# Performance work log

Measured on AMD Instinct MI355X. Metric: run time of the kernel, lower is better.

The kernel has to match this reference:

```python
import jax, jax.numpy as jnp
import numpy as np

B, NG, C, H = 16, 1024, 768, 12
CAP = 16  # fixed routing capacity in gpu_pair (8 box slots from 0 up, 8 cls slots from 15 down)


def layernorm(x, g, b, eps=1e-5):
    m = x.mean(-1, keepdims=True)
    v = jnp.mean((x - m) ** 2, axis=-1, keepdims=True)
    return (x - m) * jax.lax.rsqrt(v + eps) * g + b


def setup_inputs() -> dict:
    key = jax.random.key(0)
    ks = jax.random.split(key, 8)
    s = 0.02
    return {
        "general_token": jax.random.normal(ks[0], (B, NG, C), jnp.float32),
        "cls_token": jax.random.normal(ks[1], (B, 1, C), jnp.float32),
        "box_token": jax.random.normal(ks[2], (B, 1, C), jnp.float32),
        "w_qkv": jax.random.normal(ks[3], (3 * C, C), jnp.float32) * s,
        "w_proj": jax.random.normal(ks[4], (C, C), jnp.float32) * s,
        "b_proj": jnp.zeros((C,), jnp.float32),
        "gamma1": jnp.ones((C,), jnp.float32),
        "beta1": jnp.zeros((C,), jnp.float32),
    }


def _route(sum_a, is_box):
    """On-device replication of gpu_pair's serial CPU loop for slots 0..15.

    Tokens are processed in descending sum_attn order; box-preferred tokens fill
    slots 0,1,2,..., cls-preferred tokens fill slots 15,14,13,.... Each category's
    writer per slot is unique; on a box/cls collision the later (larger sorted
    position) write wins, matching the serial loop's overwrite semantics. Slots
    never written stay 0 (np.zeros init). Wrapped-around writes (rank >= 16) land
    outside slots 0..15 in the original and are irrelevant to the output.
    """
    ng = sum_a.shape[0]
    perm = jnp.argsort(-sum_a)                      # descending sort
    ib = is_box[perm]
    ibi = ib.astype(jnp.int32)
    box_rank = jnp.cumsum(ibi) - ibi                # exclusive prefix count of box tokens
    cls_rank = jnp.cumsum(1 - ibi) - (1 - ibi)      # exclusive prefix count of cls tokens
    j = jnp.arange(ng, dtype=jnp.int32)
    box_pos = jnp.where(ib & (box_rank < CAP), box_rank, CAP)
    cls_pos = jnp.where((~ib) & (cls_rank < CAP), (CAP - 1) - cls_rank, CAP)
    empty = jnp.full((CAP,), -1, jnp.int32)
    box_j = empty.at[box_pos].set(j, mode='drop')   # unique writer per slot
    cls_j = empty.at[cls_pos].set(j, mode='drop')
    win = jnp.maximum(box_j, cls_j)
    return jnp.where(win >= 0, perm[jnp.maximum(win, 0)], 0)


def reference(general_token, cls_token, box_token, w_qkv, w_proj, b_proj, gamma1, beta1):
    # cat order in torch: cat(cls, cat(box, general)) -> [cls, box, general]
    cat = jnp.concatenate([cls_token, box_token, general_token], axis=1)  # [B,N,C]
    Bq, N, Cq = cat.shape
    hd = Cq // H
    x = layernorm(cat, gamma1, beta1)
    qkv = (x @ w_qkv.T).reshape(Bq, N, 3, H, hd).transpose(2, 0, 3, 1, 4)
    q, k, v = qkv[0], qkv[1], qkv[2]
    attn = jnp.einsum('bhnd,bhmd->bhnm', q, k) * (hd ** -0.5)
    # raw scores between cls<->box zeroed BEFORE softmax (not -inf)
    attn = attn.at[:, :, 0, 1].set(0.0).at[:, :, 1, 0].set(0.0)
    attn = jax.nn.softmax(attn, axis=-1)
    out = jnp.einsum('bhnm,bhmd->bhnd', attn, v).transpose(0, 2, 1, 3).reshape(Bq, N, Cq)
    out = out @ w_proj.T + b_proj
    cat = cat + out  # residual (drop_path identity in eval)
    cls_t, box_t, gen = cat[:, 0:1], cat[:, 1:2], cat[:, 2:]
    cls_attn = attn[:, :, 0, 2:].mean(axis=1)  # [B, N-2]
    box_attn = attn[:, :, 1, 2:].mean(axis=1)
    idx = jax.vmap(_route)(cls_attn + box_attn, box_attn > cls_attn)  # [B,16]
    gathered = jnp.take_along_axis(gen, idx[:, :, None], axis=1)      # [B,16,C]
    cls_task_token = jnp.concatenate([cls_t, gathered[:, 0:8]], axis=1)   # [B,9,C]
    box_task_token = jnp.concatenate([box_t, gathered[:, 8:16]], axis=1)  # [B,9,C]
    return cls_task_token, box_task_token
```

## Files before the change

kernel.cpp:

```cpp
#include <hip/hip_runtime.h>
#include <math.h>

namespace {

constexpr int Bn = 16;
constexpr int NG = 1024;
constexpr int Cc = 768;
constexpr int Hh = 12;
constexpr int HD = 64;
constexpr int Nn = 1026;
constexpr int NR = 18;
constexpr int NPK = 1152;
constexpr int NCH = 24;

typedef __attribute__((ext_vector_type(8))) short short8;
typedef __attribute__((ext_vector_type(4))) float f32x4;

__device__ inline unsigned short f2bf(float f) {
  unsigned u = __float_as_uint(f);
  unsigned r = u + 0x7FFFu + ((u >> 16) & 1u);
  return (unsigned short)(r >> 16);
}

__global__ __launch_bounds__(256) void k_ln(
    const float* __restrict__ gen, const float* __restrict__ cls,
    const float* __restrict__ box, const float* __restrict__ gamma,
    const float* __restrict__ beta, float* __restrict__ x,
    unsigned short* __restrict__ xbf) {
  int blk = blockIdx.x;
  int b = blk / Nn, n = blk % Nn;
  const float* src = (n == 0) ? cls + (size_t)b * Cc
                   : (n == 1) ? box + (size_t)b * Cc
                              : gen + ((size_t)b * NG + (n - 2)) * Cc;
  int t = threadIdx.x;
  float v0 = src[t], v1 = src[t + 256], v2 = src[t + 512];
  __shared__ double red[8];
  double s = (double)v0 + (double)v1 + (double)v2;
  for (int o = 32; o > 0; o >>= 1) s += __shfl_down(s, o, 64);
  int wid = t >> 6, lid = t & 63;
  if (lid == 0) red[wid] = s;
  __syncthreads();
  if (t == 0) red[4] = (red[0] + red[1] + red[2] + red[3]) / Cc;
  __syncthreads();
  double mean = red[4];
  double d0 = (double)v0 - mean, d1 = (double)v1 - mean, d2 = (double)v2 - mean;
  double sq = d0 * d0 + d1 * d1 + d2 * d2;
  for (int o = 32; o > 0; o >>= 1) sq += __shfl_down(sq, o, 64);
  __syncthreads();
  if (lid == 0) red[wid] = sq;
  __syncthreads();
  if (t == 0) {
    double var = (red[0] + red[1] + red[2] + red[3]) / Cc;
    red[5] = 1.0 / sqrt(var + 1e-5);
  }
  __syncthreads();
  double rs = red[5];
  float* dst = x + ((size_t)b * Nn + n) * Cc;
  unsigned short* dbf = xbf + ((size_t)b * NPK + n) * Cc;
  float o0 = (float)(d0 * rs * (double)gamma[t]       + (double)beta[t]);
  float o1 = (float)(d1 * rs * (double)gamma[t + 256] + (double)beta[t + 256]);
  float o2 = (float)(d2 * rs * (double)gamma[t + 512] + (double)beta[t + 512]);
  dst[t] = o0; dst[t + 256] = o1; dst[t + 512] = o2;
  dbf[t] = f2bf(o0); dbf[t + 256] = f2bf(o1); dbf[t + 512] = f2bf(o2);
}

__global__ __launch_bounds__(256) void k_padzero(unsigned short* __restrict__ xbf) {
  constexpr int PERB = (NPK - Nn) * Cc / 2;
  int idx = blockIdx.x * 256 + threadIdx.x;
  int total = Bn * PERB;
  for (int i = idx; i < total; i += gridDim.x * 256) {
    int b = i / PERB, r = i % PERB;
    unsigned int* p = (unsigned int*)(xbf + ((size_t)b * NPK + Nn) * Cc);
    p[r] = 0u;
  }
}

__global__ __launch_bounds__(256) void k_xt(
    const unsigned short* __restrict__ xbf, unsigned short* __restrict__ xT) {
  int b = blockIdx.x, jt = blockIdx.y, ct = blockIdx.z;
  int j0 = jt * 64, c0 = ct * 64;
  __shared__ unsigned short ts[64][80];
  int t = threadIdx.x;
  #pragma unroll
  for (int l = 0; l < 2; l++) {
    int chunk = t + l * 256;
    int r = chunk >> 3, c8 = chunk & 7;
    uint4 v = *(const uint4*)(xbf + ((size_t)b * NPK + j0 + r) * Cc + c0 + c8 * 8);
    *(uint4*)&ts[r][c8 * 8] = v;
  }
  __syncthreads();
  #pragma unroll
  for (int l = 0; l < 2; l++) {
    int chunk = t + l * 256;
    int orow = chunk >> 3, j8 = chunk & 7;
    unsigned short tmp[8];
    #pragma unroll
    for (int i = 0; i < 8; i++) tmp[i] = ts[j8 * 8 + i][orow];
    *(uint4*)(xT + ((size_t)b * Cc + c0 + orow) * NPK + j0 + j8 * 8) = *(uint4*)tmp;
  }
}

__global__ __launch_bounds__(256) void k_wcvt(
    const float* __restrict__ wqkv, const float* __restrict__ wproj,
    unsigned short* __restrict__ wqb, unsigned short* __restrict__ wvb,
    unsigned short* __restrict__ wpb) {
  int i = (blockIdx.x * 256 + threadIdx.x) * 4;
  if (i >= Cc * Cc) return;
  const float* wq = wqkv;
  const float* wv = wqkv + (size_t)2 * Cc * Cc;
  float4 q = *(const float4*)(wq + i);
  float4 a = *(const float4*)(wv + i);
  float4 b = *(const float4*)(wproj + i);
  ushort4 oq, oa, ob;
  oq.x = f2bf(q.x); oq.y = f2bf(q.y); oq.z = f2bf(q.z); oq.w = f2bf(q.w);
  oa.x = f2bf(a.x); oa.y = f2bf(a.y); oa.z = f2bf(a.z); oa.w = f2bf(a.w);
  ob.x = f2bf(b.x); ob.y = f2bf(b.y); ob.z = f2bf(b.z); ob.w = f2bf(b.w);
  *(ushort4*)(wqb + i) = oq;
  *(ushort4*)(wvb + i) = oa;
  *(ushort4*)(wpb + i) = ob;
}

__global__ __launch_bounds__(256) void k_wkt(
    const float* __restrict__ wqkv, unsigned short* __restrict__ wkTb) {
  int rt = blockIdx.x, ct = blockIdx.y;
  __shared__ unsigned short ts[64][72];
  int t = threadIdx.x;
  const float* src = wqkv + (size_t)Cc * Cc;
  #pragma unroll
  for (int l = 0; l < 4; l++) {
    int idx = t + l * 256;
    int r = idx >> 4, c4 = idx & 15;
    float4 v = *(const float4*)(src + (size_t)(rt * 64 + r) * Cc + ct * 64 + c4 * 4);
    ts[r][c4 * 4 + 0] = f2bf(v.x); ts[r][c4 * 4 + 1] = f2bf(v.y);
    ts[r][c4 * 4 + 2] = f2bf(v.z); ts[r][c4 * 4 + 3] = f2bf(v.w);
  }
  __syncthreads();
  #pragma unroll
  for (int l = 0; l < 2; l++) {
    int idx = t + l * 256;
    int r2 = idx >> 3, j8 = idx & 7;
    unsigned short tmp[8];
    #pragma unroll
    for (int i = 0; i < 8; i++) tmp[i] = ts[j8 * 8 + i][r2];
    *(uint4*)(wkTb + (size_t)(ct * 64 + r2) * Cc + rt * 64 + j8 * 8) = *(uint4*)tmp;
  }
}

__global__ __launch_bounds__(256) void k_q01(
    const float* __restrict__ wqkv, const float* __restrict__ x,
    double* __restrict__ q01d) {
  int row = blockIdx.x;
  int b = row >> 1, i = row & 1;
  __shared__ float xl[Cc];
  const float* xr = x + ((size_t)b * Nn + i) * Cc;
  for (int c = threadIdx.x; c < Cc; c += 256) xl[c] = xr[c];
  __syncthreads();
  int w = threadIdx.x >> 6, lane = threadIdx.x & 63;
  int o = blockIdx.y * 4 + w;
  const float* wr = wqkv + (size_t)o * Cc + lane * 12;
  const float* xs = xl + lane * 12;
  double acc = 0;
  #pragma unroll
  for (int k = 0; k < 12; k++) acc += (double)wr[k] * (double)xs[k];
  for (int off = 32; off > 0; off >>= 1) acc += __shfl_down(acc, off, 64);
  if (lane == 0) q01d[(size_t)row * Cc + o] = acc;
}

__global__ __launch_bounds__(256) void k_u01(
    const float* __restrict__ wqkv, const double* __restrict__ q01d,
    double* __restrict__ u01d) {
  int blk = blockIdx.x;
  int h = blk % Hh; int i = (blk / Hh) & 1; int b = blk / (2 * Hh);
  __shared__ double qh[HD];
  const double* q = q01d + ((size_t)b * 2 + i) * Cc + h * HD;
  if (threadIdx.x < HD) qh[threadIdx.x] = q[threadIdx.x];
  __syncthreads();
  const float* wk = wqkv + (size_t)Cc * Cc;
  int c = blockIdx.y * 256 + threadIdx.x;
  double a0 = 0, a1 = 0, a2 = 0, a3 = 0;
  #pragma unroll 4
  for (int d = 0; d < HD; d += 4) {
    a0 += qh[d]     * (double)wk[(size_t)(h * HD + d) * Cc + c];
    a1 += qh[d + 1] * (double)wk[(size_t)(h * HD + d + 1) * Cc + c];
    a2 += qh[d + 2] * (double)wk[(size_t)(h * HD + d + 2) * Cc + c];
    a3 += qh[d + 3] * (double)wk[(size_t)(h * HD + d + 3) * Cc + c];
  }
  u01d[(((size_t)(b * 2 + i)) * Hh + h) * Cc + c] = (a0 + a1) + (a2 + a3);
}

__global__ __launch_bounds__(256) void k_r01(
    const double* __restrict__ u01d, const float* __restrict__ x,
    double* __restrict__ Ld01) {
  int b = blockIdx.x >> 1, i = blockIdx.x & 1;
  int w = threadIdx.x >> 6, lane = threadIdx.x & 63;
  for (int k = 0; k < 6; k++) {
    int p = w * 6 + k;
    int h = p >> 1, j = p & 1;
    const double* u = u01d + (((size_t)(b * 2 + i)) * Hh + h) * Cc;
    const float* xr = x + ((size_t)b * Nn + j) * Cc;
    double acc = 0;
    for (int c = lane; c < Cc; c += 64) acc += u[c] * (double)xr[c];
    for (int off = 32; off > 0; off >>= 1) acc += __shfl_down(acc, off, 64);
    if (lane == 0) Ld01[(((size_t)(b * 2 + i)) * Hh + h) * 2 + j] = acc * 0.125;
  }
}

__global__ __launch_bounds__(256) void k_rlogits(
    const double* __restrict__ u01d, const float* __restrict__ x,
    float* __restrict__ Ldp) {
  int b = blockIdx.x, jt = blockIdx.y, cch = blockIdx.z;
  int c0 = cch * 32;
  int t = threadIdx.x;
  int w = t >> 6, lane = t & 63;
  int g = w >> 1;
  int pl = ((w & 1) << 6) + lane;
  int jbase = jt * 512 + pl * 4;
  __shared__ double ut[24][32];
  __shared__ float xtT[8][512];
  #pragma unroll
  for (int l = 0; l < 3; l++) {
    int ii = t + l * 256;
    int row = ii >> 5, cc = ii & 31;
    int ig = row / 12, hh = row % 12;
    ut[row][cc] = u01d[(((size_t)(b * 2 + ig)) * Hh + hh) * Cc + c0 + cc];
  }
  double acc[12][4] = {};
  for (int s = 0; s < 4; s++) {
    __syncthreads();
    #pragma unroll
    for (int l = 0; l < 4; l++) {
      int idx = t + l * 256;
      int jl = idx >> 1, half = idx & 1;
      const float* xr = x + ((size_t)b * Nn + 2 + jt * 512 + jl) * Cc + c0 + s * 8 + half * 4;
      float4 v = *(const float4*)xr;
      xtT[half * 4 + 0][jl] = v.x;
      xtT[half * 4 + 1][jl] = v.y;
      xtT[half * 4 + 2][jl] = v.z;
      xtT[half * 4 + 3][jl] = v.w;
    }
    __syncthreads();
    #pragma unroll
    for (int cc8 = 0; cc8 < 8; cc8++) {
      int cc = s * 8 + cc8;
      float4 xv = *(const float4*)&xtT[cc8][pl * 4];
      double x0 = (double)xv.x, x1 = (double)xv.y, x2 = (double)xv.z, x3 = (double)xv.w;
      #pragma unroll
      for (int h = 0; h < 12; h++) {
        double uv = ut[g * 12 + h][cc];
        acc[h][0] += uv * x0;
        acc[h][1] += uv * x1;
        acc[h][2] += uv * x2;
        acc[h][3] += uv * x3;
      }
    }
  }
  for (int h = 0; h < 12; h++) {
    float4 o;
    o.x = (float)(acc[h][0] * 0.125);
    o.y = (float)(acc[h][1] * 0.125);
    o.z = (float)(acc[h][2] * 0.125);
    o.w = (float)(acc[h][3] * 0.125);
    *(float4*)&Ldp[(((size_t)cch * Bn + b) * 24 + g * 12 + h) * 1024 + jbase] = o;
  }
}

__global__ __launch_bounds__(256) void k_rsoftmax(
    const float* __restrict__ Ldp, const double* __restrict__ Ld01,
    double* __restrict__ Ld, unsigned short* __restrict__ Pb) {
  int blk = blockIdx.x;
  int h = blk % Hh; int i = (blk / Hh) & 1; int b = blk / (2 * Hh);
  double* row = Ld + (size_t)blk * Nn;
  unsigned short* prow = Pb + ((size_t)b * 216 + i * Hh + h) * NPK;
  int t = threadIdx.x;
  size_t poff = ((size_t)b * 24 + i * 12 + h) * 1024;
  constexpr size_t PSTRIDE = (size_t)Bn * 24 * 1024;
  double lv[5];
  int cnt = 0;
  double mx = -1e300;
  for (int j = t; j < Nn; j += 256) {
    double L;
    if (j < 2) {
      L = Ld01[(((size_t)(b * 2 + i)) * Hh + h) * 2 + j];
      if (i == 0 && j == 1) L = 0.0;
      if (i == 1 && j == 0) L = 0.0;
    } else {
      L = 0;
      #pragma unroll
      for (int p = 0; p < NCH; p++) L += (double)Ldp[(size_t)p * PSTRIDE + poff + (j - 2)];
    }
    lv[cnt++] = L;
    mx = fmax(mx, L);
  }
  __shared__ double sd[256];
  sd[t] = mx; __syncthreads();
  for (int st = 128; st > 0; st >>= 1) { if (t < st) sd[t] = fmax(sd[t], sd[t + st]); __syncthreads(); }
  mx = sd[0]; __syncthreads();
  double sum = 0;
  for (int k = 0; k < cnt; k++) { lv[k] = exp(lv[k] - mx); sum += lv[k]; }
  sd[t] = sum; __syncthreads();
  for (int st = 128; st > 0; st >>= 1) { if (t < st) sd[t] += sd[t + st]; __syncthreads(); }
  double inv = 1.0 / sd[0];
  int k = 0;
  for (int j = t; j < Nn; j += 256) {
    double p = lv[k++] * inv;
    row[j] = p;
    prow[j] = f2bf((float)p);
  }
  for (int j = Nn + t; j < NPK; j += 256) prow[j] = 0;
}

__global__ __launch_bounds__(256) void k_rsums(
    const double* __restrict__ Ld, double* __restrict__ suma,
    double* __restrict__ diffd) {
  int b = blockIdx.x;
  for (int jg = threadIdx.x; jg < NG; jg += 256) {
    int j = jg + 2;
    double cs = 0, bs = 0;
    for (int h = 0; h < Hh; h++) {
      cs += Ld[(((size_t)(b * 2 + 0)) * Hh + h) * Nn + j];
      bs += Ld[(((size_t)(b * 2 + 1)) * Hh + h) * Nn + j];
    }
    cs /= 12.0; bs /= 12.0;
    suma[(size_t)b * NG + jg] = cs + bs;
    diffd[(size_t)b * NG + jg] = bs - cs;
  }
}

__global__ __launch_bounds__(256) void k_route(
    const double* __restrict__ suma, const double* __restrict__ diffd,
    int* __restrict__ rowcat) {
  int b = blockIdx.x, t = threadIdx.x;
  __shared__ double vals[NG];
  __shared__ unsigned char flags[NG];
  __shared__ double redv[4];
  __shared__ int redi[4];
  __shared__ int blist[16], clist[16];
  __shared__ double blv[16], clv[16];
  for (int j = t; j < NG; j += 256) {
    vals[j] = suma[(size_t)b * NG + j];
    flags[j] = diffd[(size_t)b * NG + j] > 0.0 ? 1 : 0;
  }
  __syncthreads();
  int half = t >> 7;
  int lt = t & 127;
  int wv = t >> 6;
  int lane = t & 63;
  for (int s = 0; s < 16; s++) {
    double bv = -1e300; int bi = 0x7fffffff;
    #pragma unroll
    for (int k = 0; k < 8; k++) {
      int j = lt * 8 + k;
      double v = vals[j];
      if (flags[j] == half && v > bv) { bv = v; bi = j; }
    }
    for (int off = 32; off > 0; off >>= 1) {
      double ov = __shfl_down(bv, off, 64);
      int oi = __shfl_down(bi, off, 64);
      if (ov > bv || (ov == bv && oi < bi)) { bv = ov; bi = oi; }
    }
    if (lane == 0) { redv[wv] = bv; redi[wv] = bi; }
    __syncthreads();
    if (lt == 0) {
      double v0 = redv[half * 2], v1 = redv[half * 2 + 1];
      int i0 = redi[half * 2], i1 = redi[half * 2 + 1];
      if (v1 > v0 || (v1 == v0 && i1 < i0)) { v0 = v1; i0 = i1; }
      int win = (v0 > -1e299) ? i0 : -1;
      if (half) { blist[s] = win; blv[s] = v0; }
      else      { clist[s] = win; clv[s] = v0; }
      if (win >= 0) vals[win] = -1e300;
    }
    __syncthreads();
  }
  if (t < 16) {
    int s = t;
    int bc = blist[s];
    int cl = clist[15 - s];
    double bvv = blv[s], cvv = clv[15 - s];
    int win;
    if (bc < 0 && cl < 0) win = -1;
    else if (bc < 0) win = cl;
    else if (cl < 0) win = bc;
    else {
      bool boxwins = (bvv < cvv) || (bvv == cvv && bc > cl);
      win = boxwins ? bc : cl;
    }
    int tok = (win >= 0) ? win : 0;
    rowcat[b * NR + 2 + s] = tok + 2;
  }
  if (t == 0) { rowcat[b * NR + 0] = 0; rowcat[b * NR + 1] = 1; }
}

__global__ __launch_bounds__(256) void k_qg_mfma(
    const unsigned short* __restrict__ xbf, const unsigned short* __restrict__ wqb,
    const int* __restrict__ rowcat, unsigned short* __restrict__ qb) {
  int mt = blockIdx.x, ng = blockIdx.y;
  int wid = threadIdx.x >> 6, lane = threadIdx.x & 63;
  int nt = ng * 4 + wid;
  int m = lane & 15, kg = lane >> 4;
  int rowi = mt * 16 + m;
  int b = rowi >> 4, s = rowi & 15;
  int tok = rowcat[b * NR + 2 + s];
  const unsigned short* abase = xbf + ((size_t)b * NPK + tok) * Cc + kg * 8;
  const unsigned short* bbase = wqb + (size_t)(nt * 16 + m) * Cc + kg * 8;
  f32x4 acc = {0, 0, 0, 0};
  for (int k0 = 0; k0 < Cc; k0 += 32) {
    short8 a = *(const short8*)(abase + k0);
    short8 bf = *(const short8*)(bbase + k0);
    acc = __builtin_amdgcn_mfma_f32_16x16x32_bf16(a, bf, acc, 0, 0, 0);
  }
  int c = nt * 16 + m;
  #pragma unroll
  for (int r = 0; r < 4; r++) {
    int rowo = mt * 16 + kg * 4 + r;
    qb[(size_t)rowo * Cc + c] = f2bf(acc[r]);
  }
}

__global__ __launch_bounds__(256) void k_ug_mfma(
    const unsigned short* __restrict__ qb, const unsigned short* __restrict__ wkTb,
    unsigned short* __restrict__ u16b) {
  int h = blockIdx.x, mt = blockIdx.y, ngz = blockIdx.z;
  int wid = threadIdx.x >> 6, lane = threadIdx.x & 63;
  int m = lane & 15, kg = lane >> 4;
  int rowi = mt * 16 + m;
  const unsigned short* abase = qb + (size_t)rowi * Cc + h * HD + kg * 8;
  f32x4 acc[4] = {{0,0,0,0},{0,0,0,0},{0,0,0,0},{0,0,0,0}};
  #pragma unroll
  for (int k0 = 0; k0 < HD; k0 += 32) {
    short8 a = *(const short8*)(abase + k0);
    #pragma unroll
    for (int t = 0; t < 4; t++) {
      int c = ngz * 256 + (wid * 4 + t) * 16 + m;
      short8 bf = *(const short8*)(wkTb + (size_t)c * Cc + h * HD + kg * 8 + k0);
      acc[t] = __builtin_amdgcn_mfma_f32_16x16x32_bf16(a, bf, acc[t], 0, 0, 0);
    }
  }
  #pragma unroll
  for (int t = 0; t < 4; t++) {
    int c = ngz * 256 + (wid * 4 + t) * 16 + m;
    #pragma unroll
    for (int r = 0; r < 4; r++) {
      int row = mt * 16 + kg * 4 + r;
      int b = row >> 4, s = row & 15;
      u16b[((size_t)b * 192 + s * Hh + h) * Cc + c] = f2bf(acc[t][r]);
    }
  }
}

__global__ __launch_bounds__(256) void k_glogits_mfma(
    const unsigned short* __restrict__ u16b, const unsigned short* __restrict__ xbf,
    float* __restrict__ S) {
  int b = blockIdx.x, mg = blockIdx.y, nz = blockIdx.z;
  __shared__ __align__(16) unsigned short Bs[2][128 * 32];
  int t = threadIdx.x, w = t >> 6, lane = t & 63;
  int wm = w >> 1, wn = w & 1;
  int m = lane & 15, kg = lane >> 4;
  int r0 = mg * 64 + wm * 32 + m;
  const unsigned short* a0p = u16b + ((size_t)b * 192 + r0) * Cc + kg * 8;
  const unsigned short* a1p = a0p + (size_t)16 * Cc;
  int scol = lane >> 2;
  int skp = (lane & 3) * 8;
  const unsigned short* gB0 = xbf + ((size_t)b * NPK + nz * 128 + w * 32 + scol) * Cc + skp;
  const unsigned short* gB1 = gB0 + (size_t)16 * Cc;
  int lo0 = (w * 32 + scol) * 32 + skp;
  int lo1 = lo0 + 16 * 32;
  constexpr int NIT = Cc / 32;
  short8 s0 = *(const short8*)(gB0);
  short8 s1 = *(const short8*)(gB1);
  *(short8*)&Bs[0][lo0] = s0;
  *(short8*)&Bs[0][lo1] = s1;
  __syncthreads();
  f32x4 acc[2][4] = {};
  for (int it = 0; it < NIT; it++) {
    int k0 = it * 32;
    int cur = it & 1;
    short8 n0, n1;
    if (it + 1 < NIT) {
      n0 = *(const short8*)(gB0 + k0 + 32);
      n1 = *(const short8*)(gB1 + k0 + 32);
    }
    short8 a0 = *(const short8*)(a0p + k0);
    short8 a1 = *(const short8*)(a1p + k0);
    #pragma unroll
    for (int tt = 0; tt < 4; tt++) {
      int col = wn * 64 + tt * 16 + m;
      short8 bf = *(const short8*)&Bs[cur][col * 32 + kg * 8];
      acc[0][tt] = __builtin_amdgcn_mfma_f32_16x16x32_bf16(a0, bf, acc[0][tt], 0, 0, 0);
      acc[1][tt] = __builtin_amdgcn_mfma_f32_16x16x32_bf16(a1, bf, acc[1][tt], 0, 0, 0);
    }
    if (it + 1 < NIT) {
      *(short8*)&Bs[cur ^ 1][lo0] = n0;
      *(short8*)&Bs[cur ^ 1][lo1] = n1;
    }
    __syncthreads();
  }
  #pragma unroll
  for (int mt = 0; mt < 2; mt++) {
    #pragma unroll
    for (int tt = 0; tt < 4; tt++) {
      int col = nz * 128 + wn * 64 + tt * 16 + m;
      #pragma unroll
      for (int r = 0; r < 4; r++) {
        int row = mg * 64 + wm * 32 + mt * 16 + kg * 4 + r;
        S[((size_t)b * 192 + row) * NPK + col] = acc[mt][tt][r] * 0.125f;
      }
    }
  }
}

__global__ __launch_bounds__(256) void k_gsoftmax(
    const float* __restrict__ S, unsigned short* __restrict__ Pb) {
  int blk = blockIdx.x;
  int b = blk / 192, r = blk % 192;
  const float* row = S + ((size_t)b * 192 + r) * NPK;
  unsigned short* prow = Pb + ((size_t)b * 216 + 24 + r) * NPK;
  int t = threadIdx.x;
  __shared__ float sd[256];
  float mx = -1e30f;
  for (int j = t; j < Nn; j += 256) mx = fmaxf(mx, row[j]);
  sd[t] = mx; __syncthreads();
  for (int st = 128; st > 0; st >>= 1) { if (t < st) sd[t] = fmaxf(sd[t], sd[t + st]); __syncthreads(); }
  mx = sd[0]; __syncthreads();
  float sum = 0;
  for (int j = t; j < Nn; j += 256) sum += __expf(row[j] - mx);
  sd[t] = sum; __syncthreads();
  for (int st = 128; st > 0; st >>= 1) { if (t < st) sd[t] += sd[t + st]; __syncthreads(); }
  float inv = 1.0f / sd[0];
  for (int j = t; j < NPK; j += 256) {
    prow[j] = (j < Nn) ? f2bf(__expf(row[j] - mx) * inv) : (unsigned short)0;
  }
}

__global__ __launch_bounds__(256) void k_wsum_mfma(
    const unsigned short* __restrict__ Pb, const unsigned short* __restrict__ xT,
    unsigned short* __restrict__ wsumb) {
  int b = blockIdx.x, mg = blockIdx.y, nz = blockIdx.z;
  __shared__ __align__(16) unsigned short Bs[2][128 * 32];
  int t = threadIdx.x, w = t >> 6, lane = t & 63;
  int wm = w >> 1, wn = w & 1;
  int m = lane & 15, kg = lane >> 4;
  int r0 = mg * 64 + wm * 32 + m;
  int rc0 = r0 < 216 ? r0 : 215;
  int rc1 = (r0 + 16) < 216 ? (r0 + 16) : 215;
  const unsigned short* a0p = Pb + ((size_t)b * 216 + rc0) * NPK + kg * 8;
  const unsigned short* a1p = Pb + ((size_t)b * 216 + rc1) * NPK + kg * 8;
  int scol = lane >> 2;
  int skp = (lane & 3) * 8;
  const unsigned short* gB0 = xT + ((size_t)b * Cc + nz * 128 + w * 32 + scol) * NPK + skp;
  const unsigned short* gB1 = gB0 + (size_t)16 * NPK;
  int lo0 = (w * 32 + scol) * 32 + skp;
  int lo1 = lo0 + 16 * 32;
  constexpr int NIT = NPK / 32;
  short8 s0 = *(const short8*)(gB0);
  short8 s1 = *(const short8*)(gB1);
  *(short8*)&Bs[0][lo0] = s0;
  *(short8*)&Bs[0][lo1] = s1;
  __syncthreads();
  f32x4 acc[2][4] = {};
  for (int it = 0; it < NIT; it++) {
    int k0 = it * 32;
    int cur = it & 1;
    short8 n0, n1;
    if (it + 1 < NIT) {
      n0 = *(const short8*)(gB0 + k0 + 32);
      n1 = *(const short8*)(gB1 + k0 + 32);
    }
    short8 a0 = *(const short8*)(a0p + k0);
    short8 a1 = *(const short8*)(a1p + k0);
    #pragma unroll
    for (int tt = 0; tt < 4; tt++) {
      int col = wn * 64 + tt * 16 + m;
      short8 bf = *(const short8*)&Bs[cur][col * 32 + kg * 8];
      acc[0][tt] = __builtin_amdgcn_mfma_f32_16x16x32_bf16(a0, bf, acc[0][tt], 0, 0, 0);
      acc[1][tt] = __builtin_amdgcn_mfma_f32_16x16x32_bf16(a1, bf, acc[1][tt], 0, 0, 0);
    }
    if (it + 1 < NIT) {
      *(short8*)&Bs[cur ^ 1][lo0] = n0;
      *(short8*)&Bs[cur ^ 1][lo1] = n1;
    }
    __syncthreads();
  }
  #pragma unroll
  for (int mt = 0; mt < 2; mt++) {
    #pragma unroll
    for (int tt = 0; tt < 4; tt++) {
      int col = nz * 128 + wn * 64 + tt * 16 + m;
      #pragma unroll
      for (int r = 0; r < 4; r++) {
        int row = mg * 64 + wm * 32 + mt * 16 + kg * 4 + r;
        if (row < 216) wsumb[((size_t)b * 216 + row) * Cc + col] = f2bf(acc[mt][tt][r]);
      }
    }
  }
}

__global__ __launch_bounds__(256) void k_attnout_mfma(
    const unsigned short* __restrict__ wsumb, const unsigned short* __restrict__ wvb,
    unsigned short* __restrict__ aob) {
  int h = blockIdx.x, mt = blockIdx.y;
  int wid = threadIdx.x >> 6, lane = threadIdx.x & 63;
  int m = lane & 15, kg = lane >> 4;
  int row = mt * 16 + m;
  int b = row / NR, i = row % NR;
  const unsigned short* abase = wsumb + ((size_t)b * 216 + i * 12 + h) * Cc + kg * 8;
  const unsigned short* bbase = wvb + (size_t)(h * HD + wid * 16 + m) * Cc + kg * 8;
  f32x4 acc = {0, 0, 0, 0};
  for (int k0 = 0; k0 < Cc; k0 += 32) {
    short8 a = *(const short8*)(abase + k0);
    short8 bf = *(const short8*)(bbase + k0);
    acc = __builtin_amdgcn_mfma_f32_16x16x32_bf16(a, bf, acc, 0, 0, 0);
  }
  #pragma unroll
  for (int r = 0; r < 4; r++) {
    int orow = mt * 16 + kg * 4 + r;
    int ocol = h * HD + wid * 16 + m;
    aob[(size_t)orow * Cc + ocol] = f2bf(acc[r]);
  }
}

__global__ __launch_bounds__(256) void k_proj_mfma(
    const unsigned short* __restrict__ aob, const unsigned short* __restrict__ wpb,
    const float* __restrict__ bproj, const int* __restrict__ rowcat,
    const float* __restrict__ gen, const float* __restrict__ cls,
    const float* __restrict__ box, float* __restrict__ out) {
  int mt = blockIdx.x, ng = blockIdx.y;
  int wid = threadIdx.x >> 6, lane = threadIdx.x & 63;
  int nt = ng * 4 + wid;
  int m = lane & 15, kg = lane >> 4;
  const unsigned short* abase = aob + (size_t)(mt * 16 + m) * Cc + kg * 8;
  const unsigned short* bbase = wpb + (size_t)(nt * 16 + m) * Cc + kg * 8;
  f32x4 acc = {0, 0, 0, 0};
  for (int k0 = 0; k0 < Cc; k0 += 32) {
    short8 a = *(const short8*)(abase + k0);
    short8 bf = *(const short8*)(bbase + k0);
    acc = __builtin_amdgcn_mfma_f32_16x16x32_bf16(a, bf, acc, 0, 0, 0);
  }
  int c = nt * 16 + m;
  float bp = bproj[c];
  #pragma unroll
  for (int r = 0; r < 4; r++) {
    int bi = mt * 16 + kg * 4 + r;
    int b = bi / NR, i = bi % NR;
    int tok = rowcat[b * NR + i];
    const float* src = (tok == 0) ? cls + (size_t)b * Cc
                     : (tok == 1) ? box + (size_t)b * Cc
                                  : gen + ((size_t)b * NG + tok - 2) * Cc;
    float val = acc[r] + bp + src[c];
    float* dst;
    if (i == 0)       dst = out + ((size_t)b * 9 + 0) * Cc;
    else if (i == 1)  dst = out + (size_t)Bn * 9 * Cc + ((size_t)b * 9 + 0) * Cc;
    else if (i < 10)  dst = out + ((size_t)b * 9 + (i - 1)) * Cc;
    else              dst = out + (size_t)Bn * 9 * Cc + ((size_t)b * 9 + (i - 9)) * Cc;
    dst[c] = val;
  }
}

}

extern "C" void kernel_launch(void* const* d_in, const int* in_sizes, int n_in,
                              void* d_out, int out_size, void* d_ws, size_t ws_size,
                              hipStream_t stream) {
  (void)in_sizes; (void)n_in; (void)out_size; (void)ws_size;
  const float* gen   = (const float*)d_in[0];
  const float* cls   = (const float*)d_in[1];
  const float* box   = (const float*)d_in[2];
  const float* wqkv  = (const float*)d_in[3];
  const float* wproj = (const float*)d_in[4];
  const float* bproj = (const float*)d_in[5];
  const float* gamma = (const float*)d_in[6];
  const float* beta  = (const float*)d_in[7];
  float* out = (float*)d_out;

  char* ws = (char*)d_ws;
  size_t off = 0;
  auto alloc = [&](size_t bytes) { void* p = ws + off; off += (bytes + 255) & ~(size_t)255; return p; };
  float* x             = (float*)alloc((size_t)Bn * Nn * Cc * 4);
  unsigned short* xbf  = (unsigned short*)alloc((size_t)Bn * NPK * Cc * 2);
  unsigned short* xT   = (unsigned short*)alloc((size_t)Bn * Cc * NPK * 2);
  unsigned short* qb   = (unsigned short*)alloc((size_t)256 * Cc * 2);
  unsigned short* u16b = (unsigned short*)alloc((size_t)Bn * 192 * Cc * 2);
  float* S             = (float*)alloc((size_t)Bn * 192 * NPK * 4);
  unsigned short* Pb   = (unsigned short*)alloc((size_t)Bn * 216 * NPK * 2);
  unsigned short* wsumb= (unsigned short*)alloc((size_t)Bn * 216 * Cc * 2);
  unsigned short* aob  = (unsigned short*)alloc((size_t)288 * Cc * 2);
  unsigned short* wqb  = (unsigned short*)alloc((size_t)Cc * Cc * 2);
  unsigned short* wvb  = (unsigned short*)alloc((size_t)Cc * Cc * 2);
  unsigned short* wpb  = (unsigned short*)alloc((size_t)Cc * Cc * 2);
  unsigned short* wkTb = (unsigned short*)alloc((size_t)Cc * Cc * 2);
  double* q01d         = (double*)alloc((size_t)Bn * 2 * Cc * 8);
  double* u01d         = (double*)alloc((size_t)Bn * 2 * Hh * Cc * 8);
  double* Ld           = (double*)alloc((size_t)Bn * 2 * Hh * Nn * 8);
  double* Ld01         = (double*)alloc((size_t)Bn * 2 * Hh * 2 * 8);
  float* Ldp           = (float*)alloc((size_t)NCH * Bn * 24 * 1024 * 4);
  double* suma         = (double*)alloc((size_t)Bn * NG * 8);
  double* diffd        = (double*)alloc((size_t)Bn * NG * 8);
  int* rowcat          = (int*)alloc((size_t)Bn * NR * 4);

  k_ln<<<Bn * Nn, 256, 0, stream>>>(gen, cls, box, gamma, beta, x, xbf);
  k_padzero<<<96, 256, 0, stream>>>(xbf);
  k_xt<<<dim3(Bn, NPK / 64, Cc / 64), 256, 0, stream>>>(xbf, xT);
  k_wcvt<<<(Cc * Cc / 4 + 255) / 256, 256, 0, stream>>>(wqkv, wproj, wqb, wvb, wpb);
  k_wkt<<<dim3(12, 12), 256, 0, stream>>>(wqkv, wkTb);
  k_q01<<<dim3(Bn * 2, 192), 256, 0, stream>>>(wqkv, x, q01d);
  k_u01<<<dim3(Bn * 2 * Hh, 3), 256, 0, stream>>>(wqkv, q01d, u01d);
  k_r01<<<Bn * 2, 256, 0, stream>>>(u01d, x, Ld01);
  k_rlogits<<<dim3(Bn, 2, NCH), 256, 0, stream>>>(u01d, x, Ldp);
  k_rsoftmax<<<Bn * 2 * Hh, 256, 0, stream>>>(Ldp, Ld01, Ld, Pb);
  k_rsums<<<Bn, 256, 0, stream>>>(Ld, suma, diffd);
  k_route<<<Bn, 256, 0, stream>>>(suma, diffd, rowcat);
  k_qg_mfma<<<dim3(16, 12), 256, 0, stream>>>(xbf, wqb, rowcat, qb);
  k_ug_mfma<<<dim3(Hh, 16, 3), 256, 0, stream>>>(qb, wkTb, u16b);
  k_glogits_mfma<<<dim3(Bn, 3, 9), 256, 0, stream>>>(u16b, xbf, S);
  k_gsoftmax<<<Bn * 192, 256, 0, stream>>>(S, Pb);
  k_wsum_mfma<<<dim3(Bn, 4, 6), 256, 0, stream>>>(Pb, xT, wsumb);
  k_attnout_mfma<<<dim3(Hh, 18), 256, 0, stream>>>(wsumb, wvb, aob);
  k_proj_mfma<<<dim3(18, 12), 256, 0, stream>>>(aob, wpb, bproj, rowcat, gen, cls, box, out);
}
```

Measured before the change: 323.0 us.

## Merge weight-prep kernels into one launch and retile routing-logit kernel

Folds the pad-zeroing, weight bf16 conversion and K-weight transpose kernels into a single k_prep launch that dispatches on block index, removing two kernel launches. It also retiles k_rlogits: each block now covers 48 channels (NCH 24 to 16) and each thread computes 6 heads by 8 tokens instead of 12 heads by 4 tokens. The intent is to cut launch overhead, raise reuse of the staged x values and reduce the partial-sum buffer written to Ldp. The risks are higher register pressure from the 48 double accumulators and possible LDS bank conflicts from the padded 516-float xtT rows.

```diff
diff --git a/kernel.cpp b/kernel.cpp
--- a/kernel.cpp
+++ b/kernel.cpp
@@ -11,7 +11,7 @@
 constexpr int Nn = 1026;
 constexpr int NR = 18;
 constexpr int NPK = 1152;
-constexpr int NCH = 24;
+constexpr int NCH = 16;
 
 typedef __attribute__((ext_vector_type(8))) short short8;
 typedef __attribute__((ext_vector_type(4))) float f32x4;
@@ -64,14 +64,59 @@
   dbf[t] = f2bf(o0); dbf[t + 256] = f2bf(o1); dbf[t + 512] = f2bf(o2);
 }
 
-__global__ __launch_bounds__(256) void k_padzero(unsigned short* __restrict__ xbf) {
-  constexpr int PERB = (NPK - Nn) * Cc / 2;
-  int idx = blockIdx.x * 256 + threadIdx.x;
-  int total = Bn * PERB;
-  for (int i = idx; i < total; i += gridDim.x * 256) {
-    int b = i / PERB, r = i % PERB;
-    unsigned int* p = (unsigned int*)(xbf + ((size_t)b * NPK + Nn) * Cc);
-    p[r] = 0u;
+__global__ __launch_bounds__(256) void k_prep(
+    const float* __restrict__ wqkv, const float* __restrict__ wproj,
+    unsigned short* __restrict__ xbf, unsigned short* __restrict__ wqb,
+    unsigned short* __restrict__ wvb, unsigned short* __restrict__ wpb,
+    unsigned short* __restrict__ wkTb) {
+  __shared__ unsigned short ts[64][72];
+  int blk = blockIdx.x;
+  int t = threadIdx.x;
+  if (blk < 96) {
+    constexpr int PERB = (NPK - Nn) * Cc / 2;
+    int idx = blk * 256 + t;
+    int total = Bn * PERB;
+    for (int i = idx; i < total; i += 96 * 256) {
+      int b = i / PERB, r = i % PERB;
+      unsigned int* p = (unsigned int*)(xbf + ((size_t)b * NPK + Nn) * Cc);
+      p[r] = 0u;
+    }
+  } else if (blk < 672) {
+    int i = ((blk - 96) * 256 + t) * 4;
+    const float* wq = wqkv;
+    const float* wv = wqkv + (size_t)2 * Cc * Cc;
+    float4 q = *(const float4*)(wq + i);
+    float4 a = *(const float4*)(wv + i);
+    float4 b = *(const float4*)(wproj + i);
+    ushort4 oq, oa, ob;
+    oq.x = f2bf(q.x); oq.y = f2bf(q.y); oq.z = f2bf(q.z); oq.w = f2bf(q.w);
+    oa.x = f2bf(a.x); oa.y = f2bf(a.y); oa.z = f2bf(a.z); oa.w = f2bf(a.w);
+    ob.x = f2bf(b.x); ob.y = f2bf(b.y); ob.z = f2bf(b.z); ob.w = f2bf(b.w);
+    *(ushort4*)(wqb + i) = oq;
+    *(ushort4*)(wvb + i) = oa;
+    *(ushort4*)(wpb + i) = ob;
+  } else {
+    int q = blk - 672;
+    int rt = q / 12, ct = q % 12;
+    const float* src = wqkv + (size_t)Cc * Cc;
+    #pragma unroll
+    for (int l = 0; l < 4; l++) {
+      int idx = t + l * 256;
+      int r = idx >> 4, c4 = idx & 15;
+      float4 v = *(const float4*)(src + (size_t)(rt * 64 + r) * Cc + ct * 64 + c4 * 4);
+      ts[r][c4 * 4 + 0] = f2bf(v.x); ts[r][c4 * 4 + 1] = f2bf(v.y);
+      ts[r][c4 * 4 + 2] = f2bf(v.z); ts[r][c4 * 4 + 3] = f2bf(v.w);
+    }
+    __syncthreads();
+    #pragma unroll
+    for (int l = 0; l < 2; l++) {
+      int idx = t + l * 256;
+      int r2 = idx >> 3, j8 = idx & 7;
+      unsigned short tmp[8];
+      #pragma unroll
+      for (int i = 0; i < 8; i++) tmp[i] = ts[j8 * 8 + i][r2];
+      *(uint4*)(wkTb + (size_t)(ct * 64 + r2) * Cc + rt * 64 + j8 * 8) = *(uint4*)tmp;
+    }
   }
 }
 
@@ -97,52 +142,6 @@
     #pragma unroll
     for (int i = 0; i < 8; i++) tmp[i] = ts[j8 * 8 + i][orow];
     *(uint4*)(xT + ((size_t)b * Cc + c0 + orow) * NPK + j0 + j8 * 8) = *(uint4*)tmp;
-  }
-}
-
-__global__ __launch_bounds__(256) void k_wcvt(
-    const float* __restrict__ wqkv, const float* __restrict__ wproj,
-    unsigned short* __restrict__ wqb, unsigned short* __restrict__ wvb,
-    unsigned short* __restrict__ wpb) {
-  int i = (blockIdx.x * 256 + threadIdx.x) * 4;
-  if (i >= Cc * Cc) return;
-  const float* wq = wqkv;
-  const float* wv = wqkv + (size_t)2 * Cc * Cc;
-  float4 q = *(const float4*)(wq + i);
-  float4 a = *(const float4*)(wv + i);
-  float4 b = *(const float4*)(wproj + i);
-  ushort4 oq, oa, ob;
-  oq.x = f2bf(q.x); oq.y = f2bf(q.y); oq.z = f2bf(q.z); oq.w = f2bf(q.w);
-  oa.x = f2bf(a.x); oa.y = f2bf(a.y); oa.z = f2bf(a.z); oa.w = f2bf(a.w);
-  ob.x = f2bf(b.x); ob.y = f2bf(b.y); ob.z = f2bf(b.z); ob.w = f2bf(b.w);
-  *(ushort4*)(wqb + i) = oq;
-  *(ushort4*)(wvb + i) = oa;
-  *(ushort4*)(wpb + i) = ob;
-}
-
-__global__ __launch_bounds__(256) void k_wkt(
-    const float* __restrict__ wqkv, unsigned short* __restrict__ wkTb) {
-  int rt = blockIdx.x, ct = blockIdx.y;
-  __shared__ unsigned short ts[64][72];
-  int t = threadIdx.x;
-  const float* src = wqkv + (size_t)Cc * Cc;
-  #pragma unroll
-  for (int l = 0; l < 4; l++) {
-    int idx = t + l * 256;
-    int r = idx >> 4, c4 = idx & 15;
-    float4 v = *(const float4*)(src + (size_t)(rt * 64 + r) * Cc + ct * 64 + c4 * 4);
-    ts[r][c4 * 4 + 0] = f2bf(v.x); ts[r][c4 * 4 + 1] = f2bf(v.y);
-    ts[r][c4 * 4 + 2] = f2bf(v.z); ts[r][c4 * 4 + 3] = f2bf(v.w);
-  }
-  __syncthreads();
-  #pragma unroll
-  for (int l = 0; l < 2; l++) {
-    int idx = t + l * 256;
-    int r2 = idx >> 3, j8 = idx & 7;
-    unsigned short tmp[8];
-    #pragma unroll
-    for (int i = 0; i < 8; i++) tmp[i] = ts[j8 * 8 + i][r2];
-    *(uint4*)(wkTb + (size_t)(ct * 64 + r2) * Cc + rt * 64 + j8 * 8) = *(uint4*)tmp;
   }
 }
 
@@ -209,58 +208,58 @@
     const double* __restrict__ u01d, const float* __restrict__ x,
     float* __restrict__ Ldp) {
   int b = blockIdx.x, jt = blockIdx.y, cch = blockIdx.z;
-  int c0 = cch * 32;
+  int c0 = cch * 48;
   int t = threadIdx.x;
   int w = t >> 6, lane = t & 63;
   int g = w >> 1;
-  int pl = ((w & 1) << 6) + lane;
-  int jbase = jt * 512 + pl * 4;
-  __shared__ double ut[24][32];
-  __shared__ float xtT[8][512];
-  #pragma unroll
-  for (int l = 0; l < 3; l++) {
-    int ii = t + l * 256;
-    int row = ii >> 5, cc = ii & 31;
-    int ig = row / 12, hh = row % 12;
-    ut[row][cc] = u01d[(((size_t)(b * 2 + ig)) * Hh + hh) * Cc + c0 + cc];
-  }
-  double acc[12][4] = {};
-  for (int s = 0; s < 4; s++) {
+  int hh = (w & 1) * 6;
+  __shared__ double ut[24][48];
+  __shared__ __align__(16) float xtT[16][516];
+  for (int idx = t; idx < 24 * 48; idx += 256) {
+    int row = idx / 48, cc = idx % 48;
+    int ig = row / 12, hr = row % 12;
+    ut[row][cc] = u01d[(((size_t)(b * 2 + ig)) * Hh + hr) * Cc + c0 + cc];
+  }
+  double acc[6][8] = {};
+  for (int s = 0; s < 3; s++) {
+    #pragma unroll
+    for (int l = 0; l < 8; l++) {
+      int idx = t + l * 256;
+      int row = idx >> 2, c4 = idx & 3;
+      const float* xr = x + ((size_t)b * Nn + 2 + jt * 512 + row) * Cc + c0 + s * 16 + c4 * 4;
+      float4 v = *(const float4*)xr;
+      xtT[c4 * 4 + 0][row] = v.x;
+      xtT[c4 * 4 + 1][row] = v.y;
+      xtT[c4 * 4 + 2][row] = v.z;
+      xtT[c4 * 4 + 3][row] = v.w;
+    }
     __syncthreads();
-    #pragma unroll
-    for (int l = 0; l < 4; l++) {
-      int idx = t + l * 256;
-      int jl = idx >> 1, half = idx & 1;
-      const float* xr = x + ((size_t)b * Nn + 2 + jt * 512 + jl) * Cc + c0 + s * 8 + half * 4;
-      float4 v = *(const float4*)xr;
-      xtT[half * 4 + 0][jl] = v.x;
-      xtT[half * 4 + 1][jl] = v.y;
-      xtT[half * 4 + 2][jl] = v.z;
-      xtT[half * 4 + 3][jl] = v.w;
+    for (int cc = 0; cc < 16; cc++) {
+      float4 xa = *(const float4*)&xtT[cc][lane * 8];
+      float4 xb = *(const float4*)&xtT[cc][lane * 8 + 4];
+      double x0 = (double)xa.x, x1 = (double)xa.y, x2 = (double)xa.z, x3 = (double)xa.w;
+      double x4 = (double)xb.x, x5 = (double)xb.y, x6 = (double)xb.z, x7 = (double)xb.w;
+      #pragma unroll
+      for (int r = 0; r < 6; r++) {
+        double uv = ut[g * 12 + hh + r][s * 16 + cc];
+        acc[r][0] += uv * x0; acc[r][1] += uv * x1;
+        acc[r][2] += uv * x2; acc[r][3] += uv * x3;
+        acc[r][4] += uv * x4; acc[r][5] += uv * x5;
+        acc[r][6] += uv * x6; acc[r][7] += uv * x7;
+      }
     }
     __syncthreads();
-    #pragma unroll
-    for (int cc8 = 0; cc8 < 8; cc8++) {
-      int cc = s * 8 + cc8;
-      float4 xv = *(const float4*)&xtT[cc8][pl * 4];
-      double x0 = (double)xv.x, x1 = (double)xv.y, x2 = (double)xv.z, x3 = (double)xv.w;
-      #pragma unroll
-      for (int h = 0; h < 12; h++) {
-        double uv = ut[g * 12 + h][cc];
-        acc[h][0] += uv * x0;
-        acc[h][1] += uv * x1;
-        acc[h][2] += uv * x2;
-        acc[h][3] += uv * x3;
-      }
-    }
-  }
-  for (int h = 0; h < 12; h++) {
-    float4 o;
-    o.x = (float)(acc[h][0] * 0.125);
-    o.y = (float)(acc[h][1] * 0.125);
-    o.z = (float)(acc[h][2] * 0.125);
-    o.w = (float)(acc[h][3] * 0.125);
-    *(float4*)&Ldp[(((size_t)cch * Bn + b) * 24 + g * 12 + h) * 1024 + jbase] = o;
+  }
+  for (int r = 0; r < 6; r++) {
+    int rowo = g * 12 + hh + r;
+    float4 o0, o1;
+    o0.x = (float)(acc[r][0] * 0.125); o0.y = (float)(acc[r][1] * 0.125);
+    o0.z = (float)(acc[r][2] * 0.125); o0.w = (float)(acc[r][3] * 0.125);
+    o1.x = (float)(acc[r][4] * 0.125); o1.y = (float)(acc[r][5] * 0.125);
+    o1.z = (float)(acc[r][6] * 0.125); o1.w = (float)(acc[r][7] * 0.125);
+    size_t base = (((size_t)cch * Bn + b) * 24 + rowo) * 1024 + jt * 512 + lane * 8;
+    *(float4*)&Ldp[base] = o0;
+    *(float4*)&Ldp[base + 4] = o1;
   }
 }
 
@@ -697,10 +696,8 @@
   int* rowcat          = (int*)alloc((size_t)Bn * NR * 4);
 
   k_ln<<<Bn * Nn, 256, 0, stream>>>(gen, cls, box, gamma, beta, x, xbf);
-  k_padzero<<<96, 256, 0, stream>>>(xbf);
+  k_prep<<<816, 256, 0, stream>>>(wqkv, wproj, xbf, wqb, wvb, wpb, wkTb);
   k_xt<<<dim3(Bn, NPK / 64, Cc / 64), 256, 0, stream>>>(xbf, xT);
-  k_wcvt<<<(Cc * Cc / 4 + 255) / 256, 256, 0, stream>>>(wqkv, wproj, wqb, wvb, wpb);
-  k_wkt<<<dim3(12, 12), 256, 0, stream>>>(wqkv, wkTb);
   k_q01<<<dim3(Bn * 2, 192), 256, 0, stream>>>(wqkv, x, q01d);
   k_u01<<<dim3(Bn * 2 * Hh, 3), 256, 0, stream>>>(wqkv, q01d, u01d);
   k_r01<<<Bn * 2, 256, 0, stream>>>(u01d, x, Ld01);
```

Result: faster. 311.5 us (-3.6%).
